# Optimization experiments

Hardware: AMD Instinct MI355X
Metric: run time of the kernel (lower is better)

Reference implementation:

```python
import jax, jax.numpy as jnp
import numpy as np

B, T, C = 2, 2048, 2048
H, G, HS = 16, 4, 128          # n_head, n_query_groups, head_size
Q_PER_KV = H // G
SWS = 1024                      # sliding_window_size
ROPE_BASE = 10000.0


def apply_rope(x, cos, sin):
    # x: [..., T, d] with d == rope_n_elem (= head_size here); cos/sin: [T, d]
    d = x.shape[-1]
    x1, x2 = x[..., : d // 2], x[..., d // 2 :]
    rotated = jnp.concatenate((-x2, x1), axis=-1)
    return x * cos + rotated * sin


def setup_inputs() -> dict:
    key = jax.random.key(0)
    k1, k2, k3 = jax.random.split(key, 3)
    x = jax.random.normal(k1, (B, T, C), dtype=jnp.float32)
    # standard RoPE cache (litgpt-style)
    inv_freq = 1.0 / (ROPE_BASE ** (jnp.arange(0, HS, 2, dtype=jnp.float32) / HS))
    ang = jnp.outer(jnp.arange(T, dtype=jnp.float32), inv_freq)  # [T, HS/2]
    ang = jnp.concatenate((ang, ang), axis=-1)                    # [T, HS]
    cos, sin = jnp.cos(ang), jnp.sin(ang)
    W_attn = jax.random.normal(k2, ((H + 2 * G) * HS, C), dtype=jnp.float32) * 0.02
    W_proj = jax.random.normal(k3, (C, H * HS), dtype=jnp.float32) * 0.02
    return {"x": x, "cos": cos, "sin": sin, "W_attn": W_attn, "W_proj": W_proj}


def reference(x, cos, sin, W_attn, W_proj):
    # fused QKV projection: [B,T,(H+2G)*HS]
    qkv = x @ W_attn.T
    # split into groups: [B,T,G,q_per_kv+2,HS] -> [B,G,total,T,HS]
    qkv = qkv.reshape(B, T, G, Q_PER_KV + 2, HS).transpose(0, 2, 3, 1, 4)
    q = qkv[:, :, :Q_PER_KV]        # [B,G,q_per_kv,T,HS]
    k = qkv[:, :, Q_PER_KV]         # [B,G,T,HS]
    v = qkv[:, :, Q_PER_KV + 1]     # [B,G,T,HS]
    # inline RoPE (rotary_percentage=1.0 -> whole head rotated)
    q = apply_rope(q, cos, sin)
    k = apply_rope(k, cos, sin)
    # sliding-window causal mask: attend iff i-SWS < j <= i
    i = jnp.arange(T)[:, None]
    j = jnp.arange(T)[None, :]
    allowed = (j <= i) & (j > i - SWS)
    mask = jnp.where(allowed, 0.0, -jnp.inf).astype(x.dtype)  # [T,T]
    # grouped attention (k/v shared across q_per_kv heads per group, same math
    # as the torch expand+reshape)
    scale = 1.0 / np.sqrt(HS).astype(np.float32)
    scores = jnp.einsum("bgqtd,bgsd->bgqts", q, k) * scale + mask
    attn = jax.nn.softmax(scores, axis=-1)
    y = jnp.einsum("bgqts,bgsd->bgqtd", attn, v)  # [B,G,q_per_kv,T,HS]
    # [B,H,T,HS] -> [B,T,H*HS]
    y = y.reshape(B, H, T, HS).transpose(0, 2, 1, 3).reshape(B, T, H * HS)
    return y @ W_proj.T
```

## Files before the change

### kernel.cpp

```cpp
#include <hip/hip_runtime.h>
#include <hip/hip_bf16.h>
#include <cstdint>
#include <type_traits>

using bf16_t = __hip_bfloat16;
typedef __bf16 bf16x8 __attribute__((ext_vector_type(8)));
typedef float f32x4 __attribute__((ext_vector_type(4)));

typedef __attribute__((address_space(3))) uint32_t lds_u32_t;
typedef const __attribute__((address_space(1))) uint32_t glb_u32_t;

__global__ void cvt_f32_to_bf16(const float* __restrict__ in, bf16_t* __restrict__ out, int n8) {
  int stride = gridDim.x * blockDim.x;
  for (int i = blockIdx.x * blockDim.x + threadIdx.x; i < n8; i += stride) {
    const float4* p = reinterpret_cast<const float4*>(in) + (size_t)i * 2;
    float4 a = p[0];
    float4 b = p[1];
    bf16_t o[8];
    o[0] = __float2bfloat16(a.x); o[1] = __float2bfloat16(a.y);
    o[2] = __float2bfloat16(a.z); o[3] = __float2bfloat16(a.w);
    o[4] = __float2bfloat16(b.x); o[5] = __float2bfloat16(b.y);
    o[6] = __float2bfloat16(b.z); o[7] = __float2bfloat16(b.w);
    *reinterpret_cast<uint4*>(out + (size_t)i * 8) = *reinterpret_cast<const uint4*>(o);
  }
}

template <int BN, typename OutT>
__global__ __launch_bounds__(512, 2) void gemm256(const bf16_t* __restrict__ A,
                                                  const bf16_t* __restrict__ Bt,
                                                  OutT* __restrict__ C,
                                                  int M, int N, int K) {
  constexpr int JN = BN / 64;
  constexpr int BL = BN / 64;
  __shared__ __align__(16) bf16_t As[2 * 256 * 64];
  __shared__ __align__(16) bf16_t Bs[2 * BN * 64];
  const int tid = threadIdx.x;
  const int lane = tid & 63;
  const int w = tid >> 6;
  const int wm = w >> 2, wn = w & 3;
  const int lr = lane & 15, lc = lane >> 4;

  const int nwg = gridDim.x * gridDim.y;
  const int orig = blockIdx.y * gridDim.x + blockIdx.x;
  const int cpx = nwg >> 3;
  const int swz = (orig & 7) * cpx + (orig >> 3);
  const int bx = swz % gridDim.x, by = swz / gridDim.x;
  const int m0 = by * 256, n0 = bx * BN;

  const int srow = tid >> 3;
  const int scol = ((tid & 7) ^ (srow & 7)) * 8;
  const bf16_t* Asrc = A + (size_t)(m0 + srow) * K + scol;
  const bf16_t* Bsrc = Bt + (size_t)(n0 + srow) * K + scol;

  f32x4 acc[8][JN] = {};

  auto stageA = [&](int bufi, int kt) {
#pragma unroll
    for (int l = 0; l < 4; ++l)
      __builtin_amdgcn_global_load_lds(
          (glb_u32_t*)(Asrc + (size_t)kt * 64 + (size_t)l * 64 * K),
          (lds_u32_t*)(As + bufi * 16384 + l * 4096 + w * 512), 16, 0, 0);
  };
  auto stageB = [&](int bufi, int kt) {
#pragma unroll
    for (int l = 0; l < BL; ++l)
      __builtin_amdgcn_global_load_lds(
          (glb_u32_t*)(Bsrc + (size_t)kt * 64 + (size_t)l * 64 * K),
          (lds_u32_t*)(Bs + bufi * BN * 64 + l * 4096 + w * 512), 16, 0, 0);
  };

  const int nt = K >> 6;
  stageA(0, 0);
  stageB(0, 0);

  bf16x8 a[8][2], bb[JN][2];
  for (int t = 0; t < nt; ++t) {
    const int buf = t & 1;
    const char* Ab = (const char*)(As + buf * 16384);
    const char* Bb = (const char*)(Bs + buf * BN * 64);
    const bool st = (t + 1 < nt);

    auto rdA = [&](int i, int kk) {
      int R = wm * 128 + i * 16 + lr;
      return *reinterpret_cast<const bf16x8*>(
          Ab + R * 128 + ((kk * 64 + lc * 16) ^ ((R & 7) << 4)));
    };
    auto rdB = [&](int j, int kk) {
      int R = wn * (BN / 4) + j * 16 + lr;
      return *reinterpret_cast<const bf16x8*>(
          Bb + R * 128 + ((kk * 64 + lc * 16) ^ ((R & 7) << 4)));
    };

    if constexpr (BL == 3) {
      asm volatile("s_waitcnt vmcnt(3)" ::: "memory");
    } else {
      asm volatile("s_waitcnt vmcnt(2)" ::: "memory");
    }
    __builtin_amdgcn_s_barrier();
#pragma unroll
    for (int i = 0; i < 8; ++i) { a[i][0] = rdA(i, 0); a[i][1] = rdA(i, 1); }
    if (st) stageA(buf ^ 1, t + 1);

    if (st) {
      asm volatile("s_waitcnt vmcnt(4)" ::: "memory");
    } else {
      asm volatile("s_waitcnt vmcnt(0)" ::: "memory");
    }
    __builtin_amdgcn_s_barrier();
#pragma unroll
    for (int j = 0; j < JN; ++j) { bb[j][0] = rdB(j, 0); bb[j][1] = rdB(j, 1); }
    if (st) stageB(buf ^ 1, t + 1);

    __builtin_amdgcn_s_setprio(1);
#pragma unroll
    for (int i = 0; i < 8; ++i)
#pragma unroll
      for (int j = 0; j < JN; ++j) {
        acc[i][j] = __builtin_amdgcn_mfma_f32_16x16x32_bf16(a[i][0], bb[j][0], acc[i][j], 0, 0, 0);
        acc[i][j] = __builtin_amdgcn_mfma_f32_16x16x32_bf16(a[i][1], bb[j][1], acc[i][j], 0, 0, 0);
      }
    __builtin_amdgcn_s_setprio(0);
  }

#pragma unroll
  for (int i = 0; i < 8; ++i)
#pragma unroll
    for (int j = 0; j < JN; ++j) {
      int row = m0 + wm * 128 + i * 16 + lc * 4;
      int col = n0 + wn * (BN / 4) + j * 16 + lr;
#pragma unroll
      for (int r = 0; r < 4; ++r) {
        float v = acc[i][j][r];
        if constexpr (std::is_same<OutT, float>::value)
          C[(size_t)(row + r) * N + col] = v;
        else
          C[(size_t)(row + r) * N + col] = __float2bfloat16(v);
      }
    }
}

__global__ __launch_bounds__(256) void rope_scatter(const bf16_t* __restrict__ qkv,
                                                    const float* __restrict__ cosp,
                                                    const float* __restrict__ sinp,
                                                    bf16_t* __restrict__ Q,
                                                    bf16_t* __restrict__ K,
                                                    bf16_t* __restrict__ V) {
  const int row = blockIdx.x;
  const int b = row >> 11, t = row & 2047;
  const bf16_t* src = qkv + (size_t)row * 3072;
  for (int n = threadIdx.x; n < 3072; n += 256) {
    int g = n / 768;
    int r = n - g * 768;
    int slot = r >> 7;
    int d = r & 127;
    if (slot == 5) {
      V[(((size_t)(b * 4 + g)) * 2048 + t) * 128 + d] = src[n];
    } else {
      float v = __bfloat162float(src[n]);
      float other = __bfloat162float(src[n ^ 64]);
      float c = cosp[t * 128 + d];
      float s = sinp[t * 128 + d];
      float rot = (d < 64) ? -other : other;
      float res = v * c + rot * s;
      if (slot < 4) {
        int h = g * 4 + slot;
        Q[(((size_t)(b * 16 + h)) * 2048 + t) * 128 + d] =
            __float2bfloat16(res * (0.08838834764831843f * 1.4426950408889634f));
      } else {
        K[(((size_t)(b * 4 + g)) * 2048 + t) * 128 + d] = __float2bfloat16(res);
      }
    }
  }
}

__global__ void transpose_v(const bf16_t* __restrict__ V, bf16_t* __restrict__ Vt) {
  __shared__ bf16_t tile[32][33];
  const int bg = blockIdx.z;
  const int t0 = blockIdx.x * 32;
  const int d0 = blockIdx.y * 32;
  const bf16_t* src = V + (size_t)bg * 2048 * 128;
  bf16_t* dst = Vt + (size_t)bg * 128 * 2048;
#pragma unroll
  for (int i = threadIdx.y; i < 32; i += 8)
    tile[i][threadIdx.x] = src[(size_t)(t0 + i) * 128 + d0 + threadIdx.x];
  __syncthreads();
#pragma unroll
  for (int i = threadIdx.y; i < 32; i += 8)
    dst[(size_t)(d0 + i) * 2048 + t0 + threadIdx.x] = tile[threadIdx.x][i];
}

#define VROW 40
__global__ __launch_bounds__(256) void attn_swa(const bf16_t* __restrict__ Q,
                                                const bf16_t* __restrict__ K,
                                                const bf16_t* __restrict__ Vt,
                                                bf16_t* __restrict__ Y) {
  __shared__ __align__(16) bf16_t Ks[2 * 32 * 128];
  __shared__ __align__(16) bf16_t Vs[2 * 128 * VROW];

  const int tid = threadIdx.x;
  const int lane = tid & 63;
  const int w = tid >> 6;
  const int lr = lane & 15, lc = lane >> 4;
  const int b = blockIdx.z, h = blockIdx.y;
  const int g = h >> 2;

  int nseg, sx0, sx1 = 0;
  if (blockIdx.x < 16) {
    nseg = 1;
    sx0 = blockIdx.x + 16;
  } else {
    nseg = 2;
    sx0 = blockIdx.x - 16;
    sx1 = 15 - sx0;
  }

  const bf16_t* Qp = Q + ((size_t)(b * 16 + h) * 2048) * 128;
  const bf16_t* Kp = K + ((size_t)(b * 4 + g) * 2048) * 128;
  const bf16_t* Vp = Vt + ((size_t)(b * 4 + g) * 128) * 2048;

  const int kmj = tid >> 4;
  const int kmc = ((tid & 15) ^ (kmj & 7)) * 8;
  const bf16_t* Ksrc = Kp + (size_t)kmj * 128 + kmc;
  const int vd = tid >> 2, vc = tid & 3;
  const bf16_t* Vsrc = Vp + (size_t)vd * 2048 + vc * 8;
  const int vdst = vd * VROW + (vc & 1) * 16 + (vc >> 1) * 4;

  auto loadK = [&](int j0, uint4& ka, uint4& kb) {
    const bf16_t* s = Ksrc + (size_t)j0 * 128;
    ka = *reinterpret_cast<const uint4*>(s);
    kb = *reinterpret_cast<const uint4*>(s + 16 * 128);
  };
  auto writeK = [&](int bufi, uint4 ka, uint4 kb) {
    *reinterpret_cast<uint4*>(Ks + bufi * 4096 + tid * 8) = ka;
    *reinterpret_cast<uint4*>(Ks + bufi * 4096 + 2048 + tid * 8) = kb;
  };
  auto loadV = [&](int j0, uint4& a, uint4& bqv) {
    a = *reinterpret_cast<const uint4*>(Vsrc + j0);
    bqv = *reinterpret_cast<const uint4*>(Vsrc + 64 * 2048 + j0);
  };
  auto writeV = [&](int bufi, uint4 a, uint4 bqv) {
    bf16_t* p = Vs + bufi * 128 * VROW + vdst;
    *reinterpret_cast<uint2*>(p) = make_uint2(a.x, a.y);
    *reinterpret_cast<uint2*>(p + 8) = make_uint2(a.z, a.w);
    bf16_t* p1 = p + 64 * VROW;
    *reinterpret_cast<uint2*>(p1) = make_uint2(bqv.x, bqv.y);
    *reinterpret_cast<uint2*>(p1 + 8) = make_uint2(bqv.z, bqv.w);
  };

  const int kxor = (lr & 7) << 4;

  for (int sidx = 0; sidx < nseg; ++sidx) {
    const int i0b = ((sidx == 0) ? sx0 : sx1) * 64;
    const int i0 = i0b + w * 16;
    const int qrow = i0 + lr;

    bf16x8 qf[4];
#pragma unroll
    for (int kc = 0; kc < 4; ++kc)
      qf[kc] = *reinterpret_cast<const bf16x8*>(&Qp[(size_t)qrow * 128 + kc * 32 + lc * 8]);

    f32x4 o[8] = {};
    float mrun = -1e30f, lrun = 0.f;

    int lo = i0b - 1023;
    if (lo < 0) lo = 0;
    const int jstart = lo & ~31;
    const int jlast = i0b + 32;

    {
      uint4 ka, kb, va, vb;
      loadK(jstart, ka, kb);
      loadV(jstart, va, vb);
      writeK(0, ka, kb);
      writeV(0, va, vb);
    }
    __syncthreads();

    int buf = 0;
    for (int j0 = jstart; j0 <= jlast; j0 += 32) {
      const int nxt = j0 + 32;
      uint4 ka, kb, va, vb;
      const bool do_stage = (nxt <= jlast);
      if (do_stage) {
        loadK(nxt, ka, kb);
        loadV(nxt, va, vb);
      }

      const bool active = (j0 <= i0 + 15) && (j0 + 31 > i0 - 1024);
      if (active) {
        const bf16_t* Kb = Ks + buf * 4096;
        const bf16_t* Vb = Vs + buf * 128 * VROW;
        f32x4 s0 = {}, s1 = {};
        __builtin_amdgcn_s_setprio(1);
#pragma unroll
        for (int kc = 0; kc < 4; ++kc) {
          int col = ((kc * 64 + lc * 16) ^ kxor) >> 1;
          bf16x8 kf0 = *reinterpret_cast<const bf16x8*>(Kb + lr * 128 + col);
          bf16x8 kf1 = *reinterpret_cast<const bf16x8*>(Kb + (16 + lr) * 128 + col);
          s0 = __builtin_amdgcn_mfma_f32_16x16x32_bf16(kf0, qf[kc], s0, 0, 0, 0);
          s1 = __builtin_amdgcn_mfma_f32_16x16x32_bf16(kf1, qf[kc], s1, 0, 0, 0);
        }
        __builtin_amdgcn_s_setprio(0);
        bf16x8 vvf[8];
#pragma unroll
        for (int f = 0; f < 8; ++f)
          vvf[f] = *reinterpret_cast<const bf16x8*>(Vb + (f * 16 + lr) * VROW + lc * 8);

        const bool full = (j0 + 31 <= i0) && (j0 >= i0 - 1008);
        if (!full) {
#pragma unroll
          for (int r = 0; r < 4; ++r) {
            int ja = j0 + lc * 4 + r;
            int jb = ja + 16;
            bool oka = (ja <= qrow) && (ja > qrow - 1024);
            bool okb = (jb <= qrow) && (jb > qrow - 1024);
            s0[r] = oka ? s0[r] : -1e30f;
            s1[r] = okb ? s1[r] : -1e30f;
          }
        }
        float rm = fmaxf(fmaxf(fmaxf(s0[0], s0[1]), fmaxf(s0[2], s0[3])),
                         fmaxf(fmaxf(s1[0], s1[1]), fmaxf(s1[2], s1[3])));

        if (!__all(rm <= mrun + 11.5f)) {
          rm = fmaxf(rm, __shfl_xor(rm, 16));
          rm = fmaxf(rm, __shfl_xor(rm, 32));
          float mnew = fmaxf(mrun, rm);
          float alpha = exp2f(mrun - mnew);
          mrun = mnew;
          lrun *= alpha;
#pragma unroll
          for (int f = 0; f < 8; ++f)
#pragma unroll
            for (int r = 0; r < 4; ++r) o[f][r] *= alpha;
        }

        float p0[4], p1[4], ps = 0.f;
#pragma unroll
        for (int r = 0; r < 4; ++r) {
          p0[r] = exp2f(s0[r] - mrun);
          p1[r] = exp2f(s1[r] - mrun);
          ps += p0[r] + p1[r];
        }
        lrun += ps;

        bf16_t pb[8];
#pragma unroll
        for (int r = 0; r < 4; ++r) {
          pb[r] = __float2bfloat16(p0[r]);
          pb[r + 4] = __float2bfloat16(p1[r]);
        }
        bf16x8 pfrag = *reinterpret_cast<bf16x8*>(pb);

        __builtin_amdgcn_s_setprio(1);
#pragma unroll
        for (int f = 0; f < 8; ++f)
          o[f] = __builtin_amdgcn_mfma_f32_16x16x32_bf16(vvf[f], pfrag, o[f], 0, 0, 0);
        __builtin_amdgcn_s_setprio(0);
      }

      if (do_stage) {
        writeK(buf ^ 1, ka, kb);
        writeV(buf ^ 1, va, vb);
      }
      __syncthreads();
      buf ^= 1;
    }

    float lt = lrun;
    lt += __shfl_xor(lt, 16);
    lt += __shfl_xor(lt, 32);
    float inv = 1.f / lt;
#pragma unroll
    for (int f = 0; f < 8; ++f) {
      bf16_t ob[4];
#pragma unroll
      for (int r = 0; r < 4; ++r) ob[r] = __float2bfloat16(o[f][r] * inv);
      *reinterpret_cast<uint2*>(
          &Y[((size_t)(b * 2048 + qrow)) * 2048 + h * 128 + f * 16 + lc * 4]) =
          *reinterpret_cast<uint2*>(ob);
    }
  }
}

extern "C" void kernel_launch(void* const* d_in, const int* in_sizes, int n_in,
                              void* d_out, int out_size, void* d_ws, size_t ws_size,
                              hipStream_t stream) {
  const float* x = (const float*)d_in[0];
  const float* cosp = (const float*)d_in[1];
  const float* sinp = (const float*)d_in[2];
  const float* Wa = (const float*)d_in[3];
  const float* Wp = (const float*)d_in[4];
  float* out = (float*)d_out;

  bf16_t* ws = (bf16_t*)d_ws;
  bf16_t* xb = ws;
  bf16_t* wab = ws + 8388608;
  bf16_t* wpb = ws + 14680064;
  bf16_t* qkv = ws + 18874368;
  bf16_t* Q = xb;
  bf16_t* Kr = wab;
  bf16_t* V = wab + 2097152;
  bf16_t* Y = qkv;
  bf16_t* Vt = qkv + 8388608;

  cvt_f32_to_bf16<<<4096, 256, 0, stream>>>(x, xb, 1048576);
  cvt_f32_to_bf16<<<3072, 256, 0, stream>>>(Wa, wab, 786432);
  cvt_f32_to_bf16<<<2048, 256, 0, stream>>>(Wp, wpb, 524288);

  gemm256<192, bf16_t><<<dim3(16, 16), 512, 0, stream>>>(xb, wab, qkv, 4096, 3072, 2048);

  rope_scatter<<<4096, 256, 0, stream>>>(qkv, cosp, sinp, Q, Kr, V);

  transpose_v<<<dim3(64, 4, 8), dim3(32, 8), 0, stream>>>(V, Vt);

  attn_swa<<<dim3(24, 16, 2), 256, 0, stream>>>(Q, Kr, Vt, Y);

  gemm256<128, float><<<dim3(16, 16), 512, 0, stream>>>(Y, wpb, out, 4096, 2048, 2048);
}
```

Before: 212.8 us.

## Merge input casts, vectorize RoPE, and transpose V directly from QKV

Folds the three fp32-to-bf16 conversion launches into one kernel. The RoPE kernel now works on 8-element vectors, each thread handling the lo/hi rotation pair with 16-byte loads and stores, and it no longer writes an intermediate V buffer. The V transpose reads V straight from the strided QKV output instead. This cuts two launches and one full V write-plus-read, at the cost of strided, less coalesced reads in the transpose.

Result: faster. 204.0 us (-4.1%).

```diff
diff --git a/kernel.cpp b/kernel.cpp
--- a/kernel.cpp
+++ b/kernel.cpp
@@ -10,19 +10,29 @@
 typedef __attribute__((address_space(3))) uint32_t lds_u32_t;
 typedef const __attribute__((address_space(1))) uint32_t glb_u32_t;
 
-__global__ void cvt_f32_to_bf16(const float* __restrict__ in, bf16_t* __restrict__ out, int n8) {
-  int stride = gridDim.x * blockDim.x;
-  for (int i = blockIdx.x * blockDim.x + threadIdx.x; i < n8; i += stride) {
-    const float4* p = reinterpret_cast<const float4*>(in) + (size_t)i * 2;
-    float4 a = p[0];
-    float4 b = p[1];
-    bf16_t o[8];
-    o[0] = __float2bfloat16(a.x); o[1] = __float2bfloat16(a.y);
-    o[2] = __float2bfloat16(a.z); o[3] = __float2bfloat16(a.w);
-    o[4] = __float2bfloat16(b.x); o[5] = __float2bfloat16(b.y);
-    o[6] = __float2bfloat16(b.z); o[7] = __float2bfloat16(b.w);
-    *reinterpret_cast<uint4*>(out + (size_t)i * 8) = *reinterpret_cast<const uint4*>(o);
-  }
+__global__ void cvt3(const float* __restrict__ x, const float* __restrict__ wa,
+                     const float* __restrict__ wp, bf16_t* __restrict__ xb,
+                     bf16_t* __restrict__ wab, bf16_t* __restrict__ wpb) {
+  int i = blockIdx.x * blockDim.x + threadIdx.x;
+  const float* src;
+  bf16_t* dst;
+  int off;
+  if (i < 1048576) {
+    src = x; dst = xb; off = i;
+  } else if (i < 1835008) {
+    src = wa; dst = wab; off = i - 1048576;
+  } else {
+    src = wp; dst = wpb; off = i - 1835008;
+  }
+  const float4* p = reinterpret_cast<const float4*>(src) + (size_t)off * 2;
+  float4 a = p[0];
+  float4 b = p[1];
+  bf16_t o[8];
+  o[0] = __float2bfloat16(a.x); o[1] = __float2bfloat16(a.y);
+  o[2] = __float2bfloat16(a.z); o[3] = __float2bfloat16(a.w);
+  o[4] = __float2bfloat16(b.x); o[5] = __float2bfloat16(b.y);
+  o[6] = __float2bfloat16(b.z); o[7] = __float2bfloat16(b.w);
+  *reinterpret_cast<uint4*>(dst + (size_t)off * 8) = *reinterpret_cast<const uint4*>(o);
 }
 
 template <int BN, typename OutT>
@@ -139,50 +149,64 @@
     }
 }
 
-__global__ __launch_bounds__(256) void rope_scatter(const bf16_t* __restrict__ qkv,
-                                                    const float* __restrict__ cosp,
-                                                    const float* __restrict__ sinp,
-                                                    bf16_t* __restrict__ Q,
-                                                    bf16_t* __restrict__ K,
-                                                    bf16_t* __restrict__ V) {
-  const int row = blockIdx.x;
+__global__ __launch_bounds__(320) void rope_qk(const bf16_t* __restrict__ qkv,
+                                               const float* __restrict__ cosp,
+                                               const float* __restrict__ sinp,
+                                               bf16_t* __restrict__ Q,
+                                               bf16_t* __restrict__ K) {
+  const int row = blockIdx.x * 2 + (threadIdx.x >= 160 ? 1 : 0);
+  const int u = threadIdx.x >= 160 ? threadIdx.x - 160 : threadIdx.x;
   const int b = row >> 11, t = row & 2047;
-  const bf16_t* src = qkv + (size_t)row * 3072;
-  for (int n = threadIdx.x; n < 3072; n += 256) {
-    int g = n / 768;
-    int r = n - g * 768;
-    int slot = r >> 7;
-    int d = r & 127;
-    if (slot == 5) {
-      V[(((size_t)(b * 4 + g)) * 2048 + t) * 128 + d] = src[n];
-    } else {
-      float v = __bfloat162float(src[n]);
-      float other = __bfloat162float(src[n ^ 64]);
-      float c = cosp[t * 128 + d];
-      float s = sinp[t * 128 + d];
-      float rot = (d < 64) ? -other : other;
-      float res = v * c + rot * s;
-      if (slot < 4) {
-        int h = g * 4 + slot;
-        Q[(((size_t)(b * 16 + h)) * 2048 + t) * 128 + d] =
-            __float2bfloat16(res * (0.08838834764831843f * 1.4426950408889634f));
-      } else {
-        K[(((size_t)(b * 4 + g)) * 2048 + t) * 128 + d] = __float2bfloat16(res);
-      }
-    }
-  }
-}
-
-__global__ void transpose_v(const bf16_t* __restrict__ V, bf16_t* __restrict__ Vt) {
+  const int g = u / 40;
+  const int r = u - g * 40;
+  const int slot = r >> 3;
+  const int d0 = (r & 7) * 8;
+
+  const bf16_t* src = qkv + (size_t)row * 3072 + g * 768 + slot * 128 + d0;
+  short lo[8], hi[8];
+  *reinterpret_cast<uint4*>(lo) = *reinterpret_cast<const uint4*>(src);
+  *reinterpret_cast<uint4*>(hi) = *reinterpret_cast<const uint4*>(src + 64);
+  float4 c0 = *reinterpret_cast<const float4*>(cosp + t * 128 + d0);
+  float4 c1 = *reinterpret_cast<const float4*>(cosp + t * 128 + d0 + 4);
+  float4 s0 = *reinterpret_cast<const float4*>(sinp + t * 128 + d0);
+  float4 s1 = *reinterpret_cast<const float4*>(sinp + t * 128 + d0 + 4);
+  float cs[8] = {c0.x, c0.y, c0.z, c0.w, c1.x, c1.y, c1.z, c1.w};
+  float sn[8] = {s0.x, s0.y, s0.z, s0.w, s1.x, s1.y, s1.z, s1.w};
+
+  const bool isq = (slot < 4);
+  const float scale = isq ? (0.08838834764831843f * 1.4426950408889634f) : 1.0f;
+
+  bf16_t olo[8], ohi[8];
+#pragma unroll
+  for (int e = 0; e < 8; ++e) {
+    float x1 = __bfloat162float(*reinterpret_cast<const bf16_t*>(&lo[e]));
+    float x2 = __bfloat162float(*reinterpret_cast<const bf16_t*>(&hi[e]));
+    olo[e] = __float2bfloat16((x1 * cs[e] - x2 * sn[e]) * scale);
+    ohi[e] = __float2bfloat16((x2 * cs[e] + x1 * sn[e]) * scale);
+  }
+
+  bf16_t* dst;
+  if (isq) {
+    int h = g * 4 + slot;
+    dst = Q + (((size_t)(b * 16 + h)) * 2048 + t) * 128 + d0;
+  } else {
+    dst = K + (((size_t)(b * 4 + g)) * 2048 + t) * 128 + d0;
+  }
+  *reinterpret_cast<uint4*>(dst) = *reinterpret_cast<const uint4*>(olo);
+  *reinterpret_cast<uint4*>(dst + 64) = *reinterpret_cast<const uint4*>(ohi);
+}
+
+__global__ void transpose_v2(const bf16_t* __restrict__ qkv, bf16_t* __restrict__ Vt) {
   __shared__ bf16_t tile[32][33];
   const int bg = blockIdx.z;
+  const int b = bg >> 2, g = bg & 3;
   const int t0 = blockIdx.x * 32;
   const int d0 = blockIdx.y * 32;
-  const bf16_t* src = V + (size_t)bg * 2048 * 128;
+  const bf16_t* src = qkv + (size_t)b * 2048 * 3072 + g * 768 + 640;
   bf16_t* dst = Vt + (size_t)bg * 128 * 2048;
 #pragma unroll
   for (int i = threadIdx.y; i < 32; i += 8)
-    tile[i][threadIdx.x] = src[(size_t)(t0 + i) * 128 + d0 + threadIdx.x];
+    tile[i][threadIdx.x] = src[(size_t)(t0 + i) * 3072 + d0 + threadIdx.x];
   __syncthreads();
 #pragma unroll
   for (int i = threadIdx.y; i < 32; i += 8)
@@ -399,19 +423,16 @@
   bf16_t* qkv = ws + 18874368;
   bf16_t* Q = xb;
   bf16_t* Kr = wab;
-  bf16_t* V = wab + 2097152;
   bf16_t* Y = qkv;
   bf16_t* Vt = qkv + 8388608;
 
-  cvt_f32_to_bf16<<<4096, 256, 0, stream>>>(x, xb, 1048576);
-  cvt_f32_to_bf16<<<3072, 256, 0, stream>>>(Wa, wab, 786432);
-  cvt_f32_to_bf16<<<2048, 256, 0, stream>>>(Wp, wpb, 524288);
+  cvt3<<<9216, 256, 0, stream>>>(x, Wa, Wp, xb, wab, wpb);
 
   gemm256<192, bf16_t><<<dim3(16, 16), 512, 0, stream>>>(xb, wab, qkv, 4096, 3072, 2048);
 
-  rope_scatter<<<4096, 256, 0, stream>>>(qkv, cosp, sinp, Q, Kr, V);
-
-  transpose_v<<<dim3(64, 4, 8), dim3(32, 8), 0, stream>>>(V, Vt);
+  rope_qk<<<2048, 320, 0, stream>>>(qkv, cosp, sinp, Q, Kr);
+
+  transpose_v2<<<dim3(64, 4, 8), dim3(32, 8), 0, stream>>>(qkv, Vt);
 
   attn_swa<<<dim3(24, 16, 2), 256, 0, stream>>>(Q, Kr, Vt, Y);
 
```
